# Kernel optimization log

Measured on AMD Instinct MI355X. Metric: run time of the kernel, lower is better.

The kernel has to match this reference:

```python
import jax, jax.numpy as jnp
import numpy as np

B_CHUNK = 5          # hardcoded self.B in the module
GAMMA = 0.9865
BATCH, SEQ, FEAT, DIM = 8, 4000, 256, 256


def setup_inputs() -> dict:
    key = jax.random.key(0)
    ks = jax.random.split(key, 6)
    xq = jax.random.normal(ks[0], (BATCH, SEQ, FEAT), jnp.float32)
    xk = jax.random.normal(ks[1], (BATCH, SEQ, FEAT), jnp.float32)
    xv = jax.random.normal(ks[2], (BATCH, SEQ, FEAT), jnp.float32)
    scale = 1.0 / np.sqrt(FEAT).astype(np.float32)
    Wq = jax.random.normal(ks[3], (FEAT, DIM), jnp.float32) * scale
    Wk = jax.random.normal(ks[4], (FEAT, DIM), jnp.float32) * scale
    Wv = jax.random.normal(ks[5], (FEAT, DIM), jnp.float32) * scale
    return {"xq": xq, "xk": xk, "xv": xv, "Wq": Wq, "Wk": Wk, "Wv": Wv}


def reference(xq, xk, xv, Wq, Wk, Wv):
    gamma = jnp.float32(GAMMA)
    B = B_CHUNK
    b, seq, _ = xq.shape
    dim = Wq.shape[1]
    n = seq // B  # number of chunks

    # projections, chunked: [b, n, B, dim]
    Q = (xq @ Wq).reshape(b, n, B, dim)
    K = (xk @ Wk).reshape(b, n, B, dim)
    V = (xv @ Wv).reshape(b, n, B, dim)

    chunk_idx = jnp.arange(n, dtype=jnp.float32)
    # Z[i] = gamma^(B - i - 1) (per-chunk scalar, as in original)
    Z = gamma ** (jnp.float32(B) - chunk_idx - 1.0)
    Vz = V * Z[None, :, None, None]

    # intra-chunk decay matrix: L[i,j] = gamma^(j-i) for i >= j, else 0
    pos = jnp.arange(B, dtype=jnp.float32)
    L = jnp.tril(gamma ** (pos[None, :] - pos[:, None]))

    # intra-chunk term: (Q K^T * L) @ V, vectorized over all chunks
    S = jnp.einsum('bnid,bnjd->bnij', Q, K)          # [b, n, B, B]
    intra = jnp.einsum('bnij,bnjd->bnid', S * L, V)  # [b, n, B, dim]

    # cross-chunk recurrence: R[i] = K_i^T Vz_i + gamma^B R[i-1]
    # X[i-1] += Q_i @ R[i-1] * gamma^(i+1)
    Qn = jnp.moveaxis(Q, 1, 0)   # [n, b, B, dim]
    Kn = jnp.moveaxis(K, 1, 0)
    Vzn = jnp.moveaxis(Vz, 1, 0)
    gB = gamma ** B

    def step(R_prev, inp):
        qi, ki, vzi, i = inp
        cross_prev = jnp.einsum('bod,bde->boe', qi, R_prev) * gamma ** (i + 1.0)
        R_new = jnp.einsum('bod,boe->bde', ki, vzi) + gB * R_prev
        return R_new, cross_prev

    R0 = jnp.zeros((b, dim, dim), xq.dtype)
    _, ys = jax.lax.scan(step, R0, (Qn, Kn, Vzn, chunk_idx))  # ys[i] = cross for chunk i-1
    cross = jnp.concatenate([ys[1:], jnp.zeros_like(ys[:1])], axis=0)  # last chunk has no cross term
    cross = jnp.moveaxis(cross, 0, 1)  # [b, n, B, dim]

    X = intra + cross
    return X.reshape(b, seq, dim)
```

## Files before the change

### kernel.cpp

```cpp
#include <hip/hip_runtime.h>
#include <cmath>

#define GAMMA 0.9865f
#define L2G   -0.01960905f
#define BATCH 8
#define SEQ   4000
#define CSUP  25
#define GSUP  32
#define RPG   125

typedef _Float16 half8 __attribute__((ext_vector_type(8)));
typedef _Float16 half4 __attribute__((ext_vector_type(4)));
typedef float    floatx4 __attribute__((ext_vector_type(4)));

__device__ __forceinline__ float gpow(float e) { return exp2f(e * L2G); }

__global__ __launch_bounds__(256) void wt_convert(
    const float* __restrict__ Wq, const float* __restrict__ Wk, const float* __restrict__ Wv,
    _Float16* __restrict__ Wt) {
    int t = blockIdx.x * 256 + threadIdx.x;
    int mat = t >> 16, rem = t & 65535;
    int n = rem >> 8, k = rem & 255;
    const float* W = (mat == 0) ? Wq : (mat == 1) ? Wk : Wv;
    Wt[(size_t)mat * 65536 + n * 256 + k] = (_Float16)W[k * 256 + n];
}

__global__ __launch_bounds__(256, 2) void qkv_gemm_f16(
    const float* __restrict__ xq, const float* __restrict__ xk, const float* __restrict__ xv,
    const _Float16* __restrict__ WtAll,
    _Float16* __restrict__ Qb, _Float16* __restrict__ Kb, _Float16* __restrict__ Vb) {
    int op = blockIdx.y;
    const float* x = (op == 0) ? xq : (op == 1) ? xk : xv;
    const _Float16* Wt = WtAll + (size_t)op * 65536;
    _Float16* dst = (op == 0) ? Qb : (op == 1) ? Kb : Vb;

    __shared__ _Float16 Xs[2][128][40];
    __shared__ _Float16 WsT[2][256][40];

    int t = threadIdx.x;
    int lane = t & 63, wave = t >> 6;
    int ln = lane & 15, q8 = (lane >> 4) << 3, q4 = (lane >> 4) << 2;
    int row0 = blockIdx.x * 128;

    int xm = t >> 3, xk_ = (t & 7) << 2;
    int wr = t >> 2, wk = (t & 3) << 3;

    floatx4 acc[8][4] = {};
    floatx4 xn[4]; half8 wn[4];

    auto loadNext = [&](int dt) {
        int k0 = dt * 32;
#pragma unroll
        for (int i = 0; i < 4; ++i)
            xn[i] = *(const floatx4*)&x[(size_t)(row0 + xm + i * 32) * 256 + k0 + xk_];
#pragma unroll
        for (int i = 0; i < 4; ++i)
            wn[i] = *(const half8*)&Wt[(wr + i * 64) * 256 + k0 + wk];
    };
    auto writeBuf = [&](int bf) {
#pragma unroll
        for (int i = 0; i < 4; ++i) {
            half4 h; h[0] = (_Float16)xn[i][0]; h[1] = (_Float16)xn[i][1];
            h[2] = (_Float16)xn[i][2]; h[3] = (_Float16)xn[i][3];
            *(half4*)&Xs[bf][xm + i * 32][xk_] = h;
        }
#pragma unroll
        for (int i = 0; i < 4; ++i)
            *(half8*)&WsT[bf][wr + i * 64][wk] = wn[i];
    };

    loadNext(0); writeBuf(0);
    int cur = 0;
    for (int dt = 0; dt < 8; ++dt) {
        __syncthreads();
        if (dt < 7) loadNext(dt + 1);
        half8 af[8];
#pragma unroll
        for (int mi = 0; mi < 8; ++mi) af[mi] = *(const half8*)&Xs[cur][mi * 16 + ln][q8];
#pragma unroll
        for (int ni = 0; ni < 4; ++ni) {
            half8 bf = *(const half8*)&WsT[cur][(wave * 4 + ni) * 16 + ln][q8];
#pragma unroll
            for (int mi = 0; mi < 8; ++mi)
                acc[mi][ni] = __builtin_amdgcn_mfma_f32_16x16x32_f16(af[mi], bf, acc[mi][ni], 0, 0, 0);
        }
        if (dt < 7) { writeBuf(cur ^ 1); cur ^= 1; }
    }
#pragma unroll
    for (int mi = 0; mi < 8; ++mi)
#pragma unroll
        for (int ni = 0; ni < 4; ++ni)
#pragma unroll
            for (int r = 0; r < 4; ++r) {
                int row = row0 + mi * 16 + q4 + r;
                int col = (wave * 4 + ni) * 16 + ln;
                dst[(size_t)row * 256 + col] = (_Float16)acc[mi][ni][r];
            }
}

__global__ __launch_bounds__(256) void vt_transpose(
    const _Float16* __restrict__ Vb, _Float16* __restrict__ VT) {
    int es = blockIdx.x, g = blockIdx.y, b = blockIdx.z;
    int t = threadIdx.x;
    __shared__ __align__(16) _Float16 Ls[64 * 136];
#pragma unroll
    for (int i = 0; i < 4; ++i) {
        int idx = t + i * 256;
        int cp = idx >> 3, eg = idx & 7;
        half8 v = {};
        if (cp < 125)
            v = *(const half8*)&Vb[((size_t)b * SEQ + g * RPG + cp) * 256 + es * 64 + eg * 8];
        int cpg = cp >> 3, c7 = cp & 7;
#pragma unroll
        for (int z = 0; z < 8; ++z) {
            int e = eg * 8 + z;
            Ls[e * 136 + ((cpg ^ (e >> 3)) << 3) + c7] = v[z];
        }
    }
    __syncthreads();
#pragma unroll
    for (int jj = 0; jj < 4; ++jj) {
        int ee = jj * 16 + (t >> 4);
        int cpg = t & 15;
        half8 h = *(const half8*)&Ls[ee * 136 + ((cpg ^ (ee >> 3)) << 3)];
        *(half8*)&VT[(((size_t)b * 256 + es * 64 + ee) * 32 + g) * 128 + cpg * 8] = h;
    }
}

__global__ __launch_bounds__(256, 2) void chunk_states_mfma(
    const _Float16* __restrict__ Kb, const _Float16* __restrict__ Vb,
    _Float16* __restrict__ Wh) {
    int eh = blockIdx.x, g = blockIdx.y, b = blockIdx.z;
    int t = threadIdx.x, lane = t & 63, wave = t >> 6;
    int ln = lane & 15, q8 = (lane >> 4) << 3, q4 = (lane >> 4) << 2;
    __shared__ __align__(16) _Float16 Vs[32 * 136];
    __shared__ __align__(16) _Float16 Ks[32 * 264];
    size_t base_row = (size_t)b * SEQ + g * RPG;
    floatx4 acc[8][4] = {};
    for (int kt = 0; kt < 4; ++kt) {
        int r0 = kt * 32;
#pragma unroll
        for (int i = 0; i < 2; ++i) {
            int idx = t + i * 256;
            int r = idx >> 4, e8 = (idx & 15) << 3;
            half8 v = {};
            if (r0 + r < RPG) {
                v = *(const half8*)&Vb[(base_row + r0 + r) * 256 + eh * 128 + e8];
                int mloc = (r0 + r) / 5;
                float a = gpow((float)(149 - 6 * mloc));
#pragma unroll
                for (int z = 0; z < 8; ++z) v[z] = (_Float16)((float)v[z] * a);
            }
            *(half8*)&Vs[r * 136 + e8] = v;
        }
#pragma unroll
        for (int i = 0; i < 4; ++i) {
            int idx = t + i * 256;
            int r = idx >> 5, d8 = (idx & 31) << 3;
            half8 v = {};
            if (r0 + r < RPG) v = *(const half8*)&Kb[(base_row + r0 + r) * 256 + d8];
            *(half8*)&Ks[r * 264 + d8] = v;
        }
        __syncthreads();
        half8 Af[8], Bf[4];
#pragma unroll
        for (int mi = 0; mi < 8; ++mi)
#pragma unroll
            for (int j = 0; j < 8; ++j) Af[mi][j] = Vs[(q8 + j) * 136 + mi * 16 + ln];
#pragma unroll
        for (int ni = 0; ni < 4; ++ni)
#pragma unroll
            for (int j = 0; j < 8; ++j) Bf[ni][j] = Ks[(q8 + j) * 264 + wave * 64 + ni * 16 + ln];
#pragma unroll
        for (int mi = 0; mi < 8; ++mi)
#pragma unroll
            for (int ni = 0; ni < 4; ++ni)
                acc[mi][ni] = __builtin_amdgcn_mfma_f32_16x16x32_f16(Af[mi], Bf[ni], acc[mi][ni], 0, 0, 0);
        __syncthreads();
    }
    size_t ob = ((size_t)(g * 8 + b)) << 16;
#pragma unroll
    for (int mi = 0; mi < 8; ++mi)
#pragma unroll
        for (int ni = 0; ni < 4; ++ni)
#pragma unroll
            for (int r = 0; r < 4; ++r) {
                int e = eh * 128 + mi * 16 + q4 + r;
                int d = wave * 64 + ni * 16 + ln;
                Wh[ob + (size_t)e * 256 + d] = (_Float16)acc[mi][ni][r];
            }
}

__global__ __launch_bounds__(256) void state_scan(
    const _Float16* __restrict__ Wh, _Float16* __restrict__ SprevT) {
    int t = blockIdx.x * 256 + threadIdx.x;
    int b = t >> 13;
    int idx = (t & 8191) << 3;
    const float gF = gpow(150.0f);
    float s[8] = {};
    for (int g = 0; g < GSUP; ++g) {
        size_t o = (((size_t)(g * 8 + b)) << 16) + idx;
        half8 w = *(const half8*)&Wh[o];
        half8 sv;
#pragma unroll
        for (int z = 0; z < 8; ++z) { sv[z] = (_Float16)s[z]; s[z] = (float)w[z] + gF * s[z]; }
        *(half8*)&SprevT[o] = sv;
    }
}

__global__ __launch_bounds__(256) void intra_sc(
    const _Float16* __restrict__ Qb, const _Float16* __restrict__ Kb, float* __restrict__ scw) {
    int b = blockIdx.y;
    int j = blockIdx.x * 4 + (threadIdx.x >> 6);
    int lane = threadIdx.x & 63;
    size_t base = ((size_t)b * SEQ + j * 5) * 256 + lane * 4;
    half4 qv[5], kv[5];
#pragma unroll
    for (int p = 0; p < 5; ++p) {
        qv[p] = *(const half4*)&Qb[base + p * 256];
        kv[p] = *(const half4*)&Kb[base + p * 256];
    }
#pragma unroll
    for (int p = 0; p < 5; ++p)
#pragma unroll
        for (int q = 0; q <= p; ++q) {
            float s = 0.f;
#pragma unroll
            for (int z = 0; z < 4; ++z) s += (float)qv[p][z] * (float)kv[q][z];
#pragma unroll
            for (int off = 32; off; off >>= 1) s += __shfl_xor(s, off, 64);
            if (lane == 0) scw[((size_t)b * 800 + j) * 25 + p * 5 + q] = s * gpow((float)(q - p));
        }
}

__global__ __launch_bounds__(256, 2) void cross_f16(
    const _Float16* __restrict__ Qb, const _Float16* __restrict__ Kb,
    const _Float16* __restrict__ VT, const _Float16* __restrict__ SprevT,
    const float* __restrict__ scw, float* __restrict__ out) {
    int eq = blockIdx.x, g = blockIdx.y, b = blockIdx.z;
    int e0 = eq * 64;
    int t = threadIdx.x;
    int lane = t & 63, wave = t >> 6;
    int ln = lane & 15, q8 = (lane >> 4) << 3, q4 = (lane >> 4) << 2;
    int m4 = (wave >> 1) * 4;
    int c4 = (wave & 1) * 4;
    int e2 = (wave & 1) * 2;

    __shared__ __align__(16) char smem[52224];
    _Float16* QsB  = (_Float16*)smem;
    _Float16* KsB  = (_Float16*)(smem + 20480);
    _Float16* SsB  = (_Float16*)(smem + 40960);
    _Float16* VsTB = (_Float16*)smem;
    _Float16* PsB  = (_Float16*)(smem + 17408);
#define QS(bf_, m_, k_)  QsB[(bf_) * 5120 + (m_) * 40 + (k_)]
#define KS(bf_, m_, k_)  KsB[(bf_) * 5120 + (m_) * 40 + (k_)]
#define SS(bf_, m_, k_)  SsB[(bf_) * 2560 + (m_) * 40 + (k_)]
#define PS(m_, k_)  PsB[(m_) * 136 + (k_)]
#define VST(m_, k_) VsTB[(m_) * 136 + (k_)]

    size_t kvbase = (size_t)b * SEQ + g * RPG;
    size_t sb = ((size_t)(g * 8 + b)) << 16;

    int sm = t >> 2, skk = (t & 3) << 3;

    floatx4 pacc[4][4] = {};
    floatx4 acc[4][2] = {};
    half8 qn[2], kn[2], sn;
    half8 vtp[4];

    auto loadNext = [&](int dt) {
        int d0 = dt * 32;
        half8 z = {};
#pragma unroll
        for (int i = 0; i < 2; ++i) {
            int m = sm + i * 64;
            int qr = g * RPG + 5 + m;
            qn[i] = z;
            if (m < 125 && qr < SEQ) qn[i] = *(const half8*)&Qb[((size_t)b * SEQ + qr) * 256 + d0 + skk];
            kn[i] = z;
            if (m < 125) kn[i] = *(const half8*)&Kb[(kvbase + m) * 256 + d0 + skk];
        }
        sn = *(const half8*)&SprevT[sb + (size_t)(e0 + sm) * 256 + d0 + skk];
    };
    auto writeBuf = [&](int bf) {
#pragma unroll
        for (int i = 0; i < 2; ++i) {
            int m = sm + i * 64;
            *(half8*)&QS(bf, m, skk) = qn[i];
            *(half8*)&KS(bf, m, skk) = kn[i];
        }
        *(half8*)&SS(bf, sm, skk) = sn;
    };

    loadNext(0); writeBuf(0);
    int cur = 0;
    for (int dt = 0; dt < 8; ++dt) {
        __syncthreads();
        if (dt < 7) loadNext(dt + 1);
        if (dt == 7) {
            size_t vtbase = (((size_t)b * 256 + e0 + sm) * 32 + g) * 128;
#pragma unroll
            for (int j = 0; j < 4; ++j)
                vtp[j] = *(const half8*)&VT[vtbase + ((j * 4 + (t & 3)) << 3)];
        }
        half8 af[4];
#pragma unroll
        for (int mi = 0; mi < 4; ++mi) af[mi] = *(const half8*)&QS(cur, (m4 + mi) * 16 + ln, q8);
#pragma unroll
        for (int ci = 0; ci < 4; ++ci) {
            half8 bf = *(const half8*)&KS(cur, (c4 + ci) * 16 + ln, q8);
#pragma unroll
            for (int mi = 0; mi < 4; ++mi)
                pacc[mi][ci] = __builtin_amdgcn_mfma_f32_16x16x32_f16(af[mi], bf, pacc[mi][ci], 0, 0, 0);
        }
#pragma unroll
        for (int ei = 0; ei < 2; ++ei) {
            half8 bf = *(const half8*)&SS(cur, (e2 + ei) * 16 + ln, q8);
#pragma unroll
            for (int mi = 0; mi < 4; ++mi)
                acc[mi][ei] = __builtin_amdgcn_mfma_f32_16x16x32_f16(af[mi], bf, acc[mi][ei], 0, 0, 0);
        }
        if (dt < 7) { writeBuf(cur ^ 1); cur ^= 1; }
    }

#pragma unroll
    for (int mi = 0; mi < 4; ++mi)
#pragma unroll
        for (int r = 0; r < 4; ++r) {
            int rp = (m4 + mi) * 16 + q4 + r;
            int rc = rp / 5;
            float rs = 0.f;
            if (rp < 125 && !(g == GSUP - 1 && rc == CSUP - 1)) rs = gpow((float)(6 * rc + 7));
            acc[mi][0][r] *= rs;
            acc[mi][1][r] *= rs;
        }

    __syncthreads();

    {
        int sg = t & 3;
#pragma unroll
        for (int j = 0; j < 4; ++j)
            *(half8*)&VST(sm, (j * 4 + sg) << 3) = vtp[j];
    }
#pragma unroll
    for (int mi = 0; mi < 4; ++mi)
#pragma unroll
        for (int ci = 0; ci < 4; ++ci)
#pragma unroll
            for (int r = 0; r < 4; ++r) {
                int rp = (m4 + mi) * 16 + q4 + r;
                int cp = (c4 + ci) * 16 + ln;
                int rc = rp / 5, cc = cp / 5;
                float w = 0.f;
                if (rp < 125 && cp < 125 && cc <= rc && !(g == GSUP - 1 && rc == CSUP - 1))
                    w = gpow((float)(6 * (rc - cc + 1)));
                PS(rp, cp) = (_Float16)(pacc[mi][ci][r] * w);
            }
    __syncthreads();

#pragma unroll
    for (int ct = 0; ct < 4; ++ct) {
        int cp0 = ct * 32;
        half8 paf[4];
#pragma unroll
        for (int mi = 0; mi < 4; ++mi) paf[mi] = *(const half8*)&PS((m4 + mi) * 16 + ln, cp0 + q8);
#pragma unroll
        for (int ei = 0; ei < 2; ++ei) {
            half8 bv = *(const half8*)&VST((e2 + ei) * 16 + ln, cp0 + q8);
#pragma unroll
            for (int mi = 0; mi < 4; ++mi)
                acc[mi][ei] = __builtin_amdgcn_mfma_f32_16x16x32_f16(paf[mi], bv, acc[mi][ei], 0, 0, 0);
        }
    }

#pragma unroll
    for (int mi = 0; mi < 4; ++mi)
#pragma unroll
        for (int r = 0; r < 4; ++r) {
            int rp = (m4 + mi) * 16 + q4 + r;
            if (rp < 125) {
                int rc = rp / 5, pp = rp - rc * 5;
                const float* srow = scw + ((size_t)b * 800 + g * 25 + rc) * 25 + pp * 5;
                float a0 = acc[mi][0][r], a1 = acc[mi][1][r];
                for (int q = 0; q <= pp; ++q) {
                    float s = srow[q];
                    a0 += s * (float)VST(e2 * 16 + ln, rc * 5 + q);
                    a1 += s * (float)VST((e2 + 1) * 16 + ln, rc * 5 + q);
                }
                size_t orow = ((size_t)b * SEQ + g * RPG + rp) * 256;
                out[orow + e0 + e2 * 16 + ln] = a0;
                out[orow + e0 + (e2 + 1) * 16 + ln] = a1;
            }
        }
}

extern "C" void kernel_launch(void* const* d_in, const int* in_sizes, int n_in,
                              void* d_out, int out_size, void* d_ws, size_t ws_size,
                              hipStream_t stream) {
    const float* xq = (const float*)d_in[0];
    const float* xk = (const float*)d_in[1];
    const float* xv = (const float*)d_in[2];
    const float* Wq = (const float*)d_in[3];
    const float* Wk = (const float*)d_in[4];
    const float* Wv = (const float*)d_in[5];
    float* out = (float*)d_out;

    const size_t NELEM = (size_t)SEQ * BATCH * 256;
    _Float16* Qb = (_Float16*)d_ws;
    _Float16* Kb = Qb + NELEM;
    _Float16* Vb = Kb + NELEM;
    _Float16* Wt = Vb + NELEM;
    _Float16* Wh = Wt + 196608;
    _Float16* SprevT = Wh + (size_t)GSUP * BATCH * 65536;
    float* scw = (float*)(SprevT + (size_t)GSUP * BATCH * 65536);
    _Float16* VT = Wh;

    wt_convert<<<dim3(768), 256, 0, stream>>>(Wq, Wk, Wv, Wt);
    qkv_gemm_f16<<<dim3(250, 3), 256, 0, stream>>>(xq, xk, xv, Wt, Qb, Kb, Vb);
    chunk_states_mfma<<<dim3(2, 32, 8), 256, 0, stream>>>(Kb, Vb, Wh);
    state_scan<<<dim3(256), 256, 0, stream>>>(Wh, SprevT);
    vt_transpose<<<dim3(4, 32, 8), 256, 0, stream>>>(Vb, VT);
    intra_sc<<<dim3(200, 8), 256, 0, stream>>>(Qb, Kb, scw);
    cross_f16<<<dim3(4, 32, 8), 256, 0, stream>>>(Qb, Kb, VT, SprevT, scw, out);
}
```

Before: 269.1 us.

## Use 512-thread blocks in cross kernel and finer-grained prefetching state scan

The cross-chunk kernel moves from 4 waves each owning a 4x4 MFMA tile block to 8 waves, each owning one 16-row strip across all columns. This spreads the tile work over more waves to raise latency hiding, and each thread loads one Q/K vector per stage instead of two. The state scan kernel now gives each thread 4 elements instead of 8, uses twice the blocks, and prefetches the next group's state before the current update to overlap the serial load chain. The catch is that each wave reloads the K and S fragments, which adds shared-memory traffic, and register pressure rises under the 512,2 launch bounds.

After: 253.7 us. -5.8%, faster.

```diff
diff --git a/kernel.cpp b/kernel.cpp
--- a/kernel.cpp
+++ b/kernel.cpp
@@ -194,17 +194,20 @@
 __global__ __launch_bounds__(256) void state_scan(
     const _Float16* __restrict__ Wh, _Float16* __restrict__ SprevT) {
     int t = blockIdx.x * 256 + threadIdx.x;
-    int b = t >> 13;
-    int idx = (t & 8191) << 3;
+    int b = t >> 14;
+    int idx = (t & 16383) << 2;
     const float gF = gpow(150.0f);
-    float s[8] = {};
+    float s[4] = {};
+    half4 w = *(const half4*)&Wh[(((size_t)b) << 16) + idx];
     for (int g = 0; g < GSUP; ++g) {
         size_t o = (((size_t)(g * 8 + b)) << 16) + idx;
-        half8 w = *(const half8*)&Wh[o];
-        half8 sv;
-#pragma unroll
-        for (int z = 0; z < 8; ++z) { sv[z] = (_Float16)s[z]; s[z] = (float)w[z] + gF * s[z]; }
-        *(half8*)&SprevT[o] = sv;
+        half4 wn = {};
+        if (g < GSUP - 1) wn = *(const half4*)&Wh[o + (8ull << 16)];
+        half4 sv;
+#pragma unroll
+        for (int z = 0; z < 4; ++z) { sv[z] = (_Float16)s[z]; s[z] = (float)w[z] + gF * s[z]; }
+        *(half4*)&SprevT[o] = sv;
+        w = wn;
     }
 }
 
@@ -233,7 +236,7 @@
         }
 }
 
-__global__ __launch_bounds__(256, 2) void cross_f16(
+__global__ __launch_bounds__(512, 2) void cross_f16(
     const _Float16* __restrict__ Qb, const _Float16* __restrict__ Kb,
     const _Float16* __restrict__ VT, const _Float16* __restrict__ SprevT,
     const float* __restrict__ scw, float* __restrict__ out) {
@@ -242,9 +245,7 @@
     int t = threadIdx.x;
     int lane = t & 63, wave = t >> 6;
     int ln = lane & 15, q8 = (lane >> 4) << 3, q4 = (lane >> 4) << 2;
-    int m4 = (wave >> 1) * 4;
-    int c4 = (wave & 1) * 4;
-    int e2 = (wave & 1) * 2;
+    int mw = wave;
 
     __shared__ __align__(16) char smem[52224];
     _Float16* QsB  = (_Float16*)smem;
@@ -261,35 +262,28 @@
     size_t kvbase = (size_t)b * SEQ + g * RPG;
     size_t sb = ((size_t)(g * 8 + b)) << 16;
 
-    int sm = t >> 2, skk = (t & 3) << 3;
-
-    floatx4 pacc[4][4] = {};
-    floatx4 acc[4][2] = {};
-    half8 qn[2], kn[2], sn;
-    half8 vtp[4];
+    int qm = t >> 2, qk = (t & 3) << 3;
+    int vm = t >> 3, vc = t & 7;
+
+    floatx4 pacc[8] = {};
+    floatx4 acc[4] = {};
+    half8 qn, kn, sn;
+    half8 vtp[2];
 
     auto loadNext = [&](int dt) {
         int d0 = dt * 32;
         half8 z = {};
-#pragma unroll
-        for (int i = 0; i < 2; ++i) {
-            int m = sm + i * 64;
-            int qr = g * RPG + 5 + m;
-            qn[i] = z;
-            if (m < 125 && qr < SEQ) qn[i] = *(const half8*)&Qb[((size_t)b * SEQ + qr) * 256 + d0 + skk];
-            kn[i] = z;
-            if (m < 125) kn[i] = *(const half8*)&Kb[(kvbase + m) * 256 + d0 + skk];
-        }
-        sn = *(const half8*)&SprevT[sb + (size_t)(e0 + sm) * 256 + d0 + skk];
+        int qr = g * RPG + 5 + qm;
+        qn = z;
+        if (qm < 125 && qr < SEQ) qn = *(const half8*)&Qb[((size_t)b * SEQ + qr) * 256 + d0 + qk];
+        kn = z;
+        if (qm < 125) kn = *(const half8*)&Kb[(kvbase + qm) * 256 + d0 + qk];
+        if (t < 256) sn = *(const half8*)&SprevT[sb + (size_t)(e0 + (t >> 2)) * 256 + d0 + qk];
     };
     auto writeBuf = [&](int bf) {
-#pragma unroll
-        for (int i = 0; i < 2; ++i) {
-            int m = sm + i * 64;
-            *(half8*)&QS(bf, m, skk) = qn[i];
-            *(half8*)&KS(bf, m, skk) = kn[i];
-        }
-        *(half8*)&SS(bf, sm, skk) = sn;
+        *(half8*)&QS(bf, qm, qk) = qn;
+        *(half8*)&KS(bf, qm, qk) = kn;
+        if (t < 256) *(half8*)&SS(bf, t >> 2, qk) = sn;
     };
 
     loadNext(0); writeBuf(0);
@@ -298,101 +292,84 @@
         __syncthreads();
         if (dt < 7) loadNext(dt + 1);
         if (dt == 7) {
-            size_t vtbase = (((size_t)b * 256 + e0 + sm) * 32 + g) * 128;
-#pragma unroll
-            for (int j = 0; j < 4; ++j)
-                vtp[j] = *(const half8*)&VT[vtbase + ((j * 4 + (t & 3)) << 3)];
-        }
-        half8 af[4];
-#pragma unroll
-        for (int mi = 0; mi < 4; ++mi) af[mi] = *(const half8*)&QS(cur, (m4 + mi) * 16 + ln, q8);
-#pragma unroll
-        for (int ci = 0; ci < 4; ++ci) {
-            half8 bf = *(const half8*)&KS(cur, (c4 + ci) * 16 + ln, q8);
-#pragma unroll
-            for (int mi = 0; mi < 4; ++mi)
-                pacc[mi][ci] = __builtin_amdgcn_mfma_f32_16x16x32_f16(af[mi], bf, pacc[mi][ci], 0, 0, 0);
-        }
-#pragma unroll
-        for (int ei = 0; ei < 2; ++ei) {
-            half8 bf = *(const half8*)&SS(cur, (e2 + ei) * 16 + ln, q8);
-#pragma unroll
-            for (int mi = 0; mi < 4; ++mi)
-                acc[mi][ei] = __builtin_amdgcn_mfma_f32_16x16x32_f16(af[mi], bf, acc[mi][ei], 0, 0, 0);
+            size_t vtbase = (((size_t)b * 256 + e0 + vm) * 32 + g) * 128;
+            vtp[0] = *(const half8*)&VT[vtbase + vc * 8];
+            vtp[1] = *(const half8*)&VT[vtbase + (vc + 8) * 8];
+        }
+        half8 af = *(const half8*)&QS(cur, mw * 16 + ln, q8);
+#pragma unroll
+        for (int ci = 0; ci < 8; ++ci) {
+            half8 bf = *(const half8*)&KS(cur, ci * 16 + ln, q8);
+            pacc[ci] = __builtin_amdgcn_mfma_f32_16x16x32_f16(af, bf, pacc[ci], 0, 0, 0);
+        }
+#pragma unroll
+        for (int ei = 0; ei < 4; ++ei) {
+            half8 sf = *(const half8*)&SS(cur, ei * 16 + ln, q8);
+            acc[ei] = __builtin_amdgcn_mfma_f32_16x16x32_f16(af, sf, acc[ei], 0, 0, 0);
         }
         if (dt < 7) { writeBuf(cur ^ 1); cur ^= 1; }
     }
 
 #pragma unroll
-    for (int mi = 0; mi < 4; ++mi)
+    for (int r = 0; r < 4; ++r) {
+        int rp = mw * 16 + q4 + r;
+        int rc = rp / 5;
+        float rs = 0.f;
+        if (rp < 125 && !(g == GSUP - 1 && rc == CSUP - 1)) rs = gpow((float)(6 * rc + 7));
+#pragma unroll
+        for (int ei = 0; ei < 4; ++ei) acc[ei][r] *= rs;
+    }
+
+    __syncthreads();
+
+    *(half8*)&VST(vm, vc << 3) = vtp[0];
+    *(half8*)&VST(vm, (vc + 8) << 3) = vtp[1];
+#pragma unroll
+    for (int ci = 0; ci < 8; ++ci)
 #pragma unroll
         for (int r = 0; r < 4; ++r) {
-            int rp = (m4 + mi) * 16 + q4 + r;
-            int rc = rp / 5;
-            float rs = 0.f;
-            if (rp < 125 && !(g == GSUP - 1 && rc == CSUP - 1)) rs = gpow((float)(6 * rc + 7));
-            acc[mi][0][r] *= rs;
-            acc[mi][1][r] *= rs;
-        }
-
-    __syncthreads();
-
-    {
-        int sg = t & 3;
-#pragma unroll
-        for (int j = 0; j < 4; ++j)
-            *(half8*)&VST(sm, (j * 4 + sg) << 3) = vtp[j];
-    }
-#pragma unroll
-    for (int mi = 0; mi < 4; ++mi)
-#pragma unroll
-        for (int ci = 0; ci < 4; ++ci)
-#pragma unroll
-            for (int r = 0; r < 4; ++r) {
-                int rp = (m4 + mi) * 16 + q4 + r;
-                int cp = (c4 + ci) * 16 + ln;
-                int rc = rp / 5, cc = cp / 5;
-                float w = 0.f;
-                if (rp < 125 && cp < 125 && cc <= rc && !(g == GSUP - 1 && rc == CSUP - 1))
-                    w = gpow((float)(6 * (rc - cc + 1)));
-                PS(rp, cp) = (_Float16)(pacc[mi][ci][r] * w);
-            }
+            int rp = mw * 16 + q4 + r;
+            int cp = ci * 16 + ln;
+            int rc = rp / 5, cc = cp / 5;
+            float w = 0.f;
+            if (rp < 125 && cp < 125 && cc <= rc && !(g == GSUP - 1 && rc == CSUP - 1))
+                w = gpow((float)(6 * (rc - cc + 1)));
+            PS(rp, cp) = (_Float16)(pacc[ci][r] * w);
+        }
     __syncthreads();
 
 #pragma unroll
     for (int ct = 0; ct < 4; ++ct) {
         int cp0 = ct * 32;
-        half8 paf[4];
-#pragma unroll
-        for (int mi = 0; mi < 4; ++mi) paf[mi] = *(const half8*)&PS((m4 + mi) * 16 + ln, cp0 + q8);
-#pragma unroll
-        for (int ei = 0; ei < 2; ++ei) {
-            half8 bv = *(const half8*)&VST((e2 + ei) * 16 + ln, cp0 + q8);
-#pragma unroll
-            for (int mi = 0; mi < 4; ++mi)
-                acc[mi][ei] = __builtin_amdgcn_mfma_f32_16x16x32_f16(paf[mi], bv, acc[mi][ei], 0, 0, 0);
-        }
-    }
-
-#pragma unroll
-    for (int mi = 0; mi < 4; ++mi)
-#pragma unroll
-        for (int r = 0; r < 4; ++r) {
-            int rp = (m4 + mi) * 16 + q4 + r;
-            if (rp < 125) {
-                int rc = rp / 5, pp = rp - rc * 5;
-                const float* srow = scw + ((size_t)b * 800 + g * 25 + rc) * 25 + pp * 5;
-                float a0 = acc[mi][0][r], a1 = acc[mi][1][r];
-                for (int q = 0; q <= pp; ++q) {
-                    float s = srow[q];
-                    a0 += s * (float)VST(e2 * 16 + ln, rc * 5 + q);
-                    a1 += s * (float)VST((e2 + 1) * 16 + ln, rc * 5 + q);
-                }
-                size_t orow = ((size_t)b * SEQ + g * RPG + rp) * 256;
-                out[orow + e0 + e2 * 16 + ln] = a0;
-                out[orow + e0 + (e2 + 1) * 16 + ln] = a1;
+        half8 paf = *(const half8*)&PS(mw * 16 + ln, cp0 + q8);
+#pragma unroll
+        for (int ei = 0; ei < 4; ++ei) {
+            half8 bv = *(const half8*)&VST(ei * 16 + ln, cp0 + q8);
+            acc[ei] = __builtin_amdgcn_mfma_f32_16x16x32_f16(paf, bv, acc[ei], 0, 0, 0);
+        }
+    }
+
+#pragma unroll
+    for (int r = 0; r < 4; ++r) {
+        int rp = mw * 16 + q4 + r;
+        if (rp < 125) {
+            int rc = rp / 5, pp = rp - rc * 5;
+            const float* srow = scw + ((size_t)b * 800 + g * 25 + rc) * 25 + pp * 5;
+            float a[4];
+#pragma unroll
+            for (int ei = 0; ei < 4; ++ei) a[ei] = acc[ei][r];
+            for (int q = 0; q <= pp; ++q) {
+                float s = srow[q];
+#pragma unroll
+                for (int ei = 0; ei < 4; ++ei)
+                    a[ei] += s * (float)VST(ei * 16 + ln, rc * 5 + q);
             }
-        }
+            size_t orow = ((size_t)b * SEQ + g * RPG + rp) * 256;
+#pragma unroll
+            for (int ei = 0; ei < 4; ++ei)
+                out[orow + e0 + ei * 16 + ln] = a[ei];
+        }
+    }
 }
 
 extern "C" void kernel_launch(void* const* d_in, const int* in_sizes, int n_in,
@@ -419,8 +396,8 @@
     wt_convert<<<dim3(768), 256, 0, stream>>>(Wq, Wk, Wv, Wt);
     qkv_gemm_f16<<<dim3(250, 3), 256, 0, stream>>>(xq, xk, xv, Wt, Qb, Kb, Vb);
     chunk_states_mfma<<<dim3(2, 32, 8), 256, 0, stream>>>(Kb, Vb, Wh);
-    state_scan<<<dim3(256), 256, 0, stream>>>(Wh, SprevT);
+    state_scan<<<dim3(512), 256, 0, stream>>>(Wh, SprevT);
     vt_transpose<<<dim3(4, 32, 8), 256, 0, stream>>>(Vb, VT);
     intra_sc<<<dim3(200, 8), 256, 0, stream>>>(Qb, Kb, scw);
-    cross_f16<<<dim3(4, 32, 8), 256, 0, stream>>>(Qb, Kb, VT, SprevT, scw, out);
-}
+    cross_f16<<<dim3(4, 32, 8), 512, 0, stream>>>(Qb, Kb, VT, SprevT, scw, out);
+}
```
